# Performance work log

Measured on AMD Instinct MI355X. Metric: run time of the kernel, lower is better.

The kernel has to match this reference:

```python
import jax, jax.numpy as jnp
import numpy as np

DIM = 1024


def setup_inputs() -> dict:
    key = jax.random.key(0)
    ks = jax.random.split(key, 12)
    d = DIM
    B, T = 8, 4096
    s = 1.0 / np.sqrt(d)
    return {
        "x": jax.random.normal(ks[0], (B, T, d), dtype=jnp.float32),
        "u": jnp.ones((d,), dtype=jnp.float32),
        "w": jnp.ones((d,), dtype=jnp.float32),
        "tmk": jnp.ones((d,), dtype=jnp.float32),
        "tmv": jnp.ones((d,), dtype=jnp.float32),
        "tmr": jnp.ones((d,), dtype=jnp.float32),
        "Wk": jax.random.normal(ks[1], (d, d), dtype=jnp.float32) * s,
        "Wv": jax.random.normal(ks[2], (d, d), dtype=jnp.float32) * s,
        "Wr": jax.random.normal(ks[3], (d, d), dtype=jnp.float32) * s,
        "Wo": jax.random.normal(ks[4], (d, d), dtype=jnp.float32) * s,
        "bo": jnp.zeros((d,), dtype=jnp.float32),
    }


def _wkv_scan(k, v, u, w):
    # k, v: [B, T, d]; u, w: [d]
    kT = jnp.swapaxes(k, 0, 1)  # [T, B, d]
    vT = jnp.swapaxes(v, 0, 1)

    def step(carry, kv_t):
        a, b = carry
        k_t, v_t = kv_t
        q = jnp.maximum(u + k_t, w)
        e1 = jnp.exp(-w - q)
        e2 = jnp.exp(u + k_t - q)
        a = e1 * a + e2 * v_t
        b = e1 * b + e2
        return (a, b), a / b

    B, _, d = k.shape
    init = (jnp.zeros((B, d), k.dtype), jnp.zeros((B, d), k.dtype))
    _, wkvT = jax.lax.scan(step, init, (kT, vT))
    return jnp.swapaxes(wkvT, 0, 1)  # [B, T, d]


def reference(x, u, w, tmk, tmv, tmr, Wk, Wv, Wr, Wo, bo):
    # time_shift: zero-pad one step at front, drop last -> x_shifted[t] = x[t-1]
    x_sh = jnp.pad(x, ((0, 0), (1, 0), (0, 0)))[:, :-1, :]
    key = x * tmk + x_sh * (1.0 - tmk)
    value = x * tmv + x_sh * (1.0 - tmv)
    receptance = jax.nn.sigmoid(x * tmr + x_sh * (1.0 - tmr))
    # torch Linear(no bias): y = x @ W.T
    k = jnp.einsum("btd,ed->bte", key, Wk)
    v = jnp.einsum("btd,ed->bte", value, Wv)
    r = jnp.einsum("btd,ed->bte", receptance, Wr)
    wkv = _wkv_scan(k, v, u, w)
    return jnp.einsum("btd,ed->bte", wkv * r, Wo) + bo
```

## Files before the change

kernel.cpp:

```cpp
#include <hip/hip_runtime.h>

#define DIMD 1024
#define BATCH 8
#define SEQ 4096
#define TCH 64
#define NCH (SEQ / TCH)

typedef short short8 __attribute__((ext_vector_type(8)));
typedef unsigned short u16x8 __attribute__((ext_vector_type(8)));
typedef __bf16 bf16x8 __attribute__((ext_vector_type(8)));
typedef float f32x4 __attribute__((ext_vector_type(4)));

static __device__ __forceinline__ unsigned short f2bf(float f) {
    unsigned int u = __builtin_bit_cast(unsigned int, f);
    u += 0x7FFFu + ((u >> 16) & 1u);
    return (unsigned short)(u >> 16);
}
static __device__ __forceinline__ float bf2f(unsigned short s) {
    return __builtin_bit_cast(float, ((unsigned int)s) << 16);
}

__global__ void detect(const unsigned* __restrict__ xw, unsigned* __restrict__ flag) {
    if (threadIdx.x == 0 && blockIdx.x == 0) {
        int cnt = 0;
        for (int i = 0; i < 64; ++i) {
            unsigned lo = xw[i] & 0xFFFFu;
            unsigned e = (lo >> 7) & 0xFFu;
            if ((e >= 0x70u && e <= 0x8Fu) || lo == 0u) ++cnt;
        }
        *flag = (cnt >= 32) ? 1u : 0u;
    }
}

__global__ void cvt_small(const void* __restrict__ s0, const void* __restrict__ s1,
                          const void* __restrict__ s2, const void* __restrict__ s3,
                          const void* __restrict__ s4, const void* __restrict__ s5,
                          float* __restrict__ dst, const unsigned* __restrict__ flag) {
    const void* s;
    switch (blockIdx.y) {
        case 0: s = s0; break; case 1: s = s1; break; case 2: s = s2; break;
        case 3: s = s3; break; case 4: s = s4; break; default: s = s5; break;
    }
    int i = blockIdx.x * 256 + threadIdx.x;
    float v = (*flag) ? bf2f(((const unsigned short*)s)[i]) : ((const float*)s)[i];
    dst[blockIdx.y * 1024 + i] = v;
}

__global__ void cvt_W(const void* __restrict__ s0, const void* __restrict__ s1,
                      const void* __restrict__ s2, const void* __restrict__ s3,
                      unsigned short* __restrict__ dst, const unsigned* __restrict__ flag) {
    const void* s;
    switch (blockIdx.y) {
        case 0: s = s0; break; case 1: s = s1; break;
        case 2: s = s2; break; default: s = s3; break;
    }
    unsigned short* d = dst + (size_t)blockIdx.y * DIMD * DIMD;
    size_t i8 = (size_t)blockIdx.x * 256 + threadIdx.x;
    if (*flag) {
        ((u16x8*)d)[i8] = ((const u16x8*)s)[i8];
    } else {
        const float4* s4 = (const float4*)s;
        float4 a = s4[i8 * 2], b = s4[i8 * 2 + 1];
        u16x8 o;
        o[0] = f2bf(a.x); o[1] = f2bf(a.y); o[2] = f2bf(a.z); o[3] = f2bf(a.w);
        o[4] = f2bf(b.x); o[5] = f2bf(b.y); o[6] = f2bf(b.z); o[7] = f2bf(b.w);
        ((u16x8*)d)[i8] = o;
    }
}

__global__ void prep3(const void* __restrict__ xb, size_t xoff,
                      const float* __restrict__ tmk, const float* __restrict__ tmv,
                      const float* __restrict__ tmr,
                      unsigned short* __restrict__ mix3, size_t mstride,
                      const unsigned* __restrict__ flag) {
    size_t i8 = (size_t)blockIdx.x * 256 + threadIdx.x;
    int d8 = (int)(i8 & 127);
    size_t row = i8 >> 7;
    int t = (int)(row & (SEQ - 1));
    float xv[8], xs[8];
    if (*flag) {
        const unsigned short* x = (const unsigned short*)xb + xoff;
        u16x8 a = ((const u16x8*)x)[i8];
#pragma unroll
        for (int j = 0; j < 8; ++j) xv[j] = bf2f(a[j]);
        if (t > 0) {
            u16x8 b = ((const u16x8*)x)[i8 - 128];
#pragma unroll
            for (int j = 0; j < 8; ++j) xs[j] = bf2f(b[j]);
        } else {
#pragma unroll
            for (int j = 0; j < 8; ++j) xs[j] = 0.f;
        }
    } else {
        const float* x = (const float*)xb + xoff;
        const float4* x4 = (const float4*)x;
        float4 a0 = x4[i8 * 2], a1 = x4[i8 * 2 + 1];
        xv[0]=a0.x; xv[1]=a0.y; xv[2]=a0.z; xv[3]=a0.w;
        xv[4]=a1.x; xv[5]=a1.y; xv[6]=a1.z; xv[7]=a1.w;
        if (t > 0) {
            float4 b0 = x4[i8 * 2 - 256], b1 = x4[i8 * 2 - 255];
            xs[0]=b0.x; xs[1]=b0.y; xs[2]=b0.z; xs[3]=b0.w;
            xs[4]=b1.x; xs[5]=b1.y; xs[6]=b1.z; xs[7]=b1.w;
        } else {
#pragma unroll
            for (int j = 0; j < 8; ++j) xs[j] = 0.f;
        }
    }
    const float4* k4 = (const float4*)tmk;
    const float4* v4 = (const float4*)tmv;
    const float4* r4 = (const float4*)tmr;
    float4 mk0 = k4[d8*2], mk1 = k4[d8*2+1];
    float4 mv0 = v4[d8*2], mv1 = v4[d8*2+1];
    float4 mr0 = r4[d8*2], mr1 = r4[d8*2+1];
    float mk[8] = {mk0.x,mk0.y,mk0.z,mk0.w, mk1.x,mk1.y,mk1.z,mk1.w};
    float mv[8] = {mv0.x,mv0.y,mv0.z,mv0.w, mv1.x,mv1.y,mv1.z,mv1.w};
    float mr[8] = {mr0.x,mr0.y,mr0.z,mr0.w, mr1.x,mr1.y,mr1.z,mr1.w};
    u16x8 ok, ov, orr;
#pragma unroll
    for (int j = 0; j < 8; ++j) {
        float dxy = xv[j] - xs[j];
        ok[j] = f2bf(xs[j] + mk[j] * dxy);
        ov[j] = f2bf(xs[j] + mv[j] * dxy);
        float r = xs[j] + mr[j] * dxy;
        orr[j] = f2bf(1.f / (1.f + __expf(-r)));
    }
    ((u16x8*)(mix3))[i8] = ok;
    ((u16x8*)(mix3 + mstride))[i8] = ov;
    ((u16x8*)(mix3 + 2 * mstride))[i8] = orr;
}

__global__ __launch_bounds__(256) void gemm_fused(
    const unsigned short* __restrict__ Aall,
    const unsigned short* __restrict__ Wall,
    const float* __restrict__ biasf,
    void* __restrict__ Cout, size_t coff,
    int M, int nx, int force_bf16, const unsigned* __restrict__ flag)
{
    __shared__ unsigned short sA[128 * 64];
    __shared__ unsigned short sB[128 * 64];

    const int tid = threadIdx.x;
    const int lane = tid & 63;
    const int wv = tid >> 6;
    const int wm = (wv >> 1) * 64;
    const int wn = (wv & 1) * 64;
    const int l15 = lane & 15;
    const int qd = lane >> 4;

    const int id = blockIdx.x;
    const int cls = id & 7;
    const int sub = id >> 3;
    const int bx = sub % nx;
    const int by = cls + 8 * (sub / nx);
    const int which = bx >> 3;
    const unsigned short* A  = Aall + (size_t)which * M * DIMD;
    const unsigned short* Wp = Wall + (size_t)which * DIMD * DIMD;
    const size_t row0 = (size_t)by * 128;
    const size_t col0 = (size_t)(bx & 7) * 128;

    f32x4 acc[4][4];
#pragma unroll
    for (int i = 0; i < 4; ++i)
#pragma unroll
        for (int j = 0; j < 4; ++j)
            acc[i][j] = {0.f, 0.f, 0.f, 0.f};

    for (int k0 = 0; k0 < DIMD; k0 += 64) {
#pragma unroll
        for (int i = 0; i < 4; ++i) {
            int c = i * 256 + tid;
            int row = c >> 3;
            int jj = c & 7;
            int kA = ((jj ^ (row & 7)) * 8);
            __builtin_amdgcn_global_load_lds(
                (const __attribute__((address_space(1))) void*)(A + (row0 + row) * (size_t)DIMD + k0 + kA),
                (__attribute__((address_space(3))) void*)(sA + c * 8), 16, 0, 0);
            __builtin_amdgcn_global_load_lds(
                (const __attribute__((address_space(1))) void*)(Wp + (col0 + row) * (size_t)DIMD + k0 + kA),
                (__attribute__((address_space(3))) void*)(sB + c * 8), 16, 0, 0);
        }
        __syncthreads();

#pragma unroll
        for (int kh = 0; kh < 2; ++kh) {
            short8 af[4], bfr[4];
#pragma unroll
            for (int mt = 0; mt < 4; ++mt) {
                int r = wm + mt * 16 + l15;
                int j = (kh * 4 + qd) ^ (r & 7);
                af[mt] = *(const short8*)(sA + r * 64 + j * 8);
            }
#pragma unroll
            for (int nt = 0; nt < 4; ++nt) {
                int r = wn + nt * 16 + l15;
                int j = (kh * 4 + qd) ^ (r & 7);
                bfr[nt] = *(const short8*)(sB + r * 64 + j * 8);
            }
#pragma unroll
            for (int mt = 0; mt < 4; ++mt)
#pragma unroll
                for (int nt = 0; nt < 4; ++nt)
                    acc[mt][nt] = __builtin_amdgcn_mfma_f32_16x16x32_bf16(
                        __builtin_bit_cast(bf16x8, af[mt]),
                        __builtin_bit_cast(bf16x8, bfr[nt]),
                        acc[mt][nt], 0, 0, 0);
        }
        __syncthreads();
    }

    const bool wb16 = force_bf16 || (*flag != 0u);
    const size_t cbase = coff + (size_t)which * M * DIMD;
#pragma unroll
    for (int nt = 0; nt < 4; ++nt) {
        size_t gc = col0 + wn + nt * 16 + l15;
        float bv = biasf ? biasf[gc] : 0.f;
#pragma unroll
        for (int mt = 0; mt < 4; ++mt) {
#pragma unroll
            for (int i = 0; i < 4; ++i) {
                size_t gr = row0 + wm + mt * 16 + qd * 4 + i;
                float vvl = acc[mt][nt][i] + bv;
                size_t idx = cbase + gr * (size_t)DIMD + gc;
                if (wb16) ((unsigned short*)Cout)[idx] = f2bf(vvl);
                else      ((float*)Cout)[idx] = vvl;
            }
        }
    }
}

__global__ void wkv_pass1(const unsigned short* __restrict__ kk,
                          const unsigned short* __restrict__ vv,
                          const float* __restrict__ uf, const float* __restrict__ wf,
                          float* __restrict__ aloc, float* __restrict__ bloc,
                          float* __restrict__ pp, int nchan)
{
    int e = blockIdx.x * 256 + threadIdx.x;
    int b = blockIdx.y, c = blockIdx.z;
    float uu = uf[e], ww = wf[e];
    size_t base = ((size_t)(b * SEQ + c * TCH)) * DIMD + e;
    float a = 0.f, bb = 0.f, P = 1.f;
    for (int t = 0; t < TCH; ++t) {
        float kt = bf2f(kk[base + (size_t)t * DIMD]);
        float vt = bf2f(vv[base + (size_t)t * DIMD]);
        float q = fmaxf(uu + kt, ww);
        float e1 = __expf(fminf(-ww - q, 60.f));
        float e2 = __expf(uu + kt - q);
        a = e1 * a + e2 * vt;
        bb = e1 * bb + e2;
        P *= e1;
    }
    P = fminf(fmaxf(P, 0.f), 1e30f);
    size_t si = (size_t)c * nchan + b * DIMD + e;
    aloc[si] = a; bloc[si] = bb; pp[si] = P;
}

__global__ void wkv_pass2(const float* __restrict__ aloc, const float* __restrict__ bloc,
                          const float* __restrict__ pp,
                          float* __restrict__ ain, float* __restrict__ bin, int nchan)
{
    int ch = blockIdx.x * 256 + threadIdx.x;
    float a = 0.f, b = 0.f;
    for (int c = 0; c < NCH; ++c) {
        size_t si = (size_t)c * nchan + ch;
        ain[si] = a; bin[si] = b;
        float P = pp[si];
        a = fmaf(P, a, aloc[si]);
        b = fmaf(P, b, bloc[si]);
    }
}

__global__ void wkv_pass3(const unsigned short* __restrict__ kk,
                          const unsigned short* __restrict__ vv,
                          const unsigned short* __restrict__ rr,
                          const float* __restrict__ uf, const float* __restrict__ wf,
                          const float* __restrict__ ain, const float* __restrict__ bin,
                          unsigned short* __restrict__ ao, int nchan)
{
    int e = blockIdx.x * 256 + threadIdx.x;
    int b = blockIdx.y, c = blockIdx.z;
    float uu = uf[e], ww = wf[e];
    size_t base = ((size_t)(b * SEQ + c * TCH)) * DIMD + e;
    size_t si = (size_t)c * nchan + b * DIMD + e;
    float a = ain[si], bb = bin[si];
    for (int t = 0; t < TCH; ++t) {
        size_t gi = base + (size_t)t * DIMD;
        float kt = bf2f(kk[gi]);
        float vt = bf2f(vv[gi]);
        float q = fmaxf(uu + kt, ww);
        float e1 = __expf(fminf(-ww - q, 60.f));
        float e2 = __expf(uu + kt - q);
        a = e1 * a + e2 * vt;
        bb = e1 * bb + e2;
        float wkv = a / fmaxf(bb, 1e-38f);
        float rv = bf2f(rr[gi]);
        ao[gi] = f2bf(wkv * rv);
    }
}

extern "C" void kernel_launch(void* const* d_in, const int* in_sizes, int n_in,
                              void* d_out, int out_size, void* d_ws, size_t ws_size,
                              hipStream_t stream) {
    const void* x   = d_in[0];
    const void* u   = d_in[1];
    const void* w   = d_in[2];
    const void* tmk = d_in[3];
    const void* tmv = d_in[4];
    const void* tmr = d_in[5];
    const void* Wk  = d_in[6];
    const void* Wv  = d_in[7];
    const void* Wr  = d_in[8];
    const void* Wo  = d_in[9];
    const void* bo  = d_in[10];
    (void)in_sizes; (void)n_in; (void)out_size;

    const size_t MB = 1ull << 20;
    int nb;
    if      (ws_size >= 432 * MB) nb = 8;
    else if (ws_size >= 124 * MB) nb = 2;
    else                          nb = 1;
    const int ngroups = BATCH / nb;
    const size_t Mg = (size_t)nb * SEQ;
    const int nchan = nb * DIMD;

    char* ws = (char*)d_ws;
    unsigned* flag = (unsigned*)(ws);
    float* smallf  = (float*)(ws + 64 * 1024);
    unsigned short* Wb = (unsigned short*)(ws + 1 * MB);
    unsigned short* mix3 = (unsigned short*)(ws + 16 * MB);
    size_t matB = Mg * DIMD * sizeof(unsigned short);
    unsigned short* kvr = (unsigned short*)((char*)mix3 + 3 * matB);
    char* sc = (char*)kvr + 3 * matB;
    size_t scanB = (size_t)NCH * nchan * sizeof(float);
    float* aloc = (float*)(sc + 0 * scanB);
    float* bloc = (float*)(sc + 1 * scanB);
    float* pp   = (float*)(sc + 2 * scanB);
    float* ain  = (float*)(sc + 3 * scanB);
    float* bin  = (float*)(sc + 4 * scanB);

    float* uf   = smallf + 0 * 1024;
    float* wf   = smallf + 1 * 1024;
    float* tmkf = smallf + 2 * 1024;
    float* tmvf = smallf + 3 * 1024;
    float* tmrf = smallf + 4 * 1024;
    float* bof  = smallf + 5 * 1024;
    unsigned short* Wob = Wb + 3ull * DIMD * DIMD;

    detect<<<1, 64, 0, stream>>>((const unsigned*)x, flag);
    cvt_small<<<dim3(4, 6), 256, 0, stream>>>(u, w, tmk, tmv, tmr, bo, smallf, flag);
    cvt_W<<<dim3(512, 4), 256, 0, stream>>>(Wk, Wv, Wr, Wo, Wb, flag);

    const size_t mstride = Mg * DIMD;
    unsigned short* kk  = kvr;
    unsigned short* vvb = kvr + mstride;
    unsigned short* rrb = kvr + 2 * mstride;
    const int ny = (int)(Mg / 128);
    dim3 gScan(DIMD / 256, nb, NCH);

    for (int g = 0; g < ngroups; ++g) {
        size_t xoff = (size_t)g * Mg * DIMD;

        prep3<<<(int)(Mg * DIMD / 8 / 256), 256, 0, stream>>>(
            x, xoff, tmkf, tmvf, tmrf, mix3, mstride, flag);
        gemm_fused<<<24 * ny, 256, 0, stream>>>(
            mix3, Wb, nullptr, kvr, 0, (int)Mg, 24, 1, flag);

        wkv_pass1<<<gScan, 256, 0, stream>>>(kk, vvb, uf, wf, aloc, bloc, pp, nchan);
        wkv_pass2<<<nchan / 256, 256, 0, stream>>>(aloc, bloc, pp, ain, bin, nchan);
        wkv_pass3<<<gScan, 256, 0, stream>>>(kk, vvb, rrb, uf, wf, ain, bin, kk, nchan);

        gemm_fused<<<8 * ny, 256, 0, stream>>>(
            kk, Wob, bof, d_out, xoff, (int)Mg, 8, 0, flag);
    }
}
```

Measured before the change: 811.8 us.

## Rewrite GEMM as 256x256 tile, 8-wave, double-buffered pipelined kernel

```diff
diff --git a/kernel.cpp b/kernel.cpp
--- a/kernel.cpp
+++ b/kernel.cpp
@@ -129,21 +129,75 @@
     ((u16x8*)(mix3 + 2 * mstride))[i8] = orr;
 }
 
-__global__ __launch_bounds__(256) void gemm_fused(
+
+static __device__ __forceinline__ void stage_half(
+    const unsigned short* __restrict__ g, unsigned short* l, int tid)
+{
+#pragma unroll
+    for (int ld = 0; ld < 2; ++ld) {
+        int c = ld * 512 + tid;
+        int row = c >> 3;
+        int jj = c & 7;
+        int kA = (jj ^ (row & 7)) * 8;
+        __builtin_amdgcn_global_load_lds(
+            (const __attribute__((address_space(1))) void*)(g + (size_t)row * DIMD + kA),
+            (__attribute__((address_space(3))) void*)(l + c * 8), 16, 0, 0);
+    }
+}
+
+#define SA_L(buf, h) (lds + (buf) * 16384 + (h) * 8192)
+#define SB_L(buf, h) (lds + 32768 + (buf) * 16384 + (h) * 8192)
+#define STA(buf, h, t) stage_half(A + (row0 + (h) * 128) * DIMD + (t) * 64, SA_L(buf, h), tid)
+#define STB(buf, h, t) stage_half(Wp + (col0 + (h) * 128) * DIMD + (t) * 64, SB_L(buf, h), tid)
+
+#define PH(Q, BUF, STAGES, TAIL)                                                   \
+    {                                                                              \
+        const unsigned short* sAb = lds + (BUF) * 16384;                           \
+        const unsigned short* sBb = lds + 32768 + (BUF) * 16384;                   \
+        short8 af[2][2];                                                           \
+        if ((Q) == 0) {                                                            \
+            _Pragma("unroll") for (int nt = 0; nt < 4; ++nt)                       \
+            _Pragma("unroll") for (int kh = 0; kh < 2; ++kh) {                     \
+                int r = wn + nt * 16 + l15;                                        \
+                int j = (kh * 4 + qd) ^ (r & 7);                                   \
+                bfr[nt][kh] = *(const short8*)(sBb + r * 64 + j * 8);              \
+            }                                                                      \
+        }                                                                          \
+        _Pragma("unroll") for (int m2 = 0; m2 < 2; ++m2)                           \
+        _Pragma("unroll") for (int kh = 0; kh < 2; ++kh) {                         \
+            int r = wm + ((Q) * 2 + m2) * 16 + l15;                                \
+            int j = (kh * 4 + qd) ^ (r & 7);                                       \
+            af[m2][kh] = *(const short8*)(sAb + r * 64 + j * 8);                   \
+        }                                                                          \
+        STAGES;                                                                    \
+        asm volatile("s_barrier" ::: "memory");                                    \
+        __builtin_amdgcn_s_setprio(1);                                             \
+        _Pragma("unroll") for (int m2 = 0; m2 < 2; ++m2)                           \
+        _Pragma("unroll") for (int nt = 0; nt < 4; ++nt)                           \
+        _Pragma("unroll") for (int kh = 0; kh < 2; ++kh)                           \
+            acc[(Q) * 2 + m2][nt] = __builtin_amdgcn_mfma_f32_16x16x32_bf16(       \
+                __builtin_bit_cast(bf16x8, af[m2][kh]),                            \
+                __builtin_bit_cast(bf16x8, bfr[nt][kh]),                           \
+                acc[(Q) * 2 + m2][nt], 0, 0, 0);                                   \
+        __builtin_amdgcn_s_setprio(0);                                             \
+        TAIL;                                                                      \
+        asm volatile("s_barrier" ::: "memory");                                    \
+    }
+
+__global__ __launch_bounds__(512, 2) void gemm_fused(
     const unsigned short* __restrict__ Aall,
     const unsigned short* __restrict__ Wall,
     const float* __restrict__ biasf,
     void* __restrict__ Cout, size_t coff,
     int M, int nx, int force_bf16, const unsigned* __restrict__ flag)
 {
-    __shared__ unsigned short sA[128 * 64];
-    __shared__ unsigned short sB[128 * 64];
+    __shared__ unsigned short lds[65536];
 
     const int tid = threadIdx.x;
     const int lane = tid & 63;
     const int wv = tid >> 6;
-    const int wm = (wv >> 1) * 64;
-    const int wn = (wv & 1) * 64;
+    const int wm = (wv >> 2) * 128;
+    const int wn = (wv & 3) * 64;
     const int l15 = lane & 15;
     const int qd = lane >> 4;
 
@@ -152,77 +206,89 @@
     const int sub = id >> 3;
     const int bx = sub % nx;
     const int by = cls + 8 * (sub / nx);
-    const int which = bx >> 3;
+    const int which = bx >> 2;
     const unsigned short* A  = Aall + (size_t)which * M * DIMD;
     const unsigned short* Wp = Wall + (size_t)which * DIMD * DIMD;
-    const size_t row0 = (size_t)by * 128;
-    const size_t col0 = (size_t)(bx & 7) * 128;
-
-    f32x4 acc[4][4];
-#pragma unroll
-    for (int i = 0; i < 4; ++i)
+    const size_t row0 = (size_t)by * 256;
+    const size_t col0 = (size_t)(bx & 3) * 256;
+
+    f32x4 acc[8][4];
+#pragma unroll
+    for (int i = 0; i < 8; ++i)
 #pragma unroll
         for (int j = 0; j < 4; ++j)
             acc[i][j] = {0.f, 0.f, 0.f, 0.f};
 
-    for (int k0 = 0; k0 < DIMD; k0 += 64) {
-#pragma unroll
-        for (int i = 0; i < 4; ++i) {
-            int c = i * 256 + tid;
-            int row = c >> 3;
-            int jj = c & 7;
-            int kA = ((jj ^ (row & 7)) * 8);
-            __builtin_amdgcn_global_load_lds(
-                (const __attribute__((address_space(1))) void*)(A + (row0 + row) * (size_t)DIMD + k0 + kA),
-                (__attribute__((address_space(3))) void*)(sA + c * 8), 16, 0, 0);
-            __builtin_amdgcn_global_load_lds(
-                (const __attribute__((address_space(1))) void*)(Wp + (col0 + row) * (size_t)DIMD + k0 + kA),
-                (__attribute__((address_space(3))) void*)(sB + c * 8), 16, 0, 0);
-        }
-        __syncthreads();
-
-#pragma unroll
-        for (int kh = 0; kh < 2; ++kh) {
-            short8 af[4], bfr[4];
-#pragma unroll
-            for (int mt = 0; mt < 4; ++mt) {
-                int r = wm + mt * 16 + l15;
-                int j = (kh * 4 + qd) ^ (r & 7);
-                af[mt] = *(const short8*)(sA + r * 64 + j * 8);
-            }
-#pragma unroll
-            for (int nt = 0; nt < 4; ++nt) {
-                int r = wn + nt * 16 + l15;
-                int j = (kh * 4 + qd) ^ (r & 7);
-                bfr[nt] = *(const short8*)(sB + r * 64 + j * 8);
-            }
-#pragma unroll
-            for (int mt = 0; mt < 4; ++mt)
-#pragma unroll
-                for (int nt = 0; nt < 4; ++nt)
-                    acc[mt][nt] = __builtin_amdgcn_mfma_f32_16x16x32_bf16(
-                        __builtin_bit_cast(bf16x8, af[mt]),
-                        __builtin_bit_cast(bf16x8, bfr[nt]),
-                        acc[mt][nt], 0, 0, 0);
-        }
-        __syncthreads();
+    short8 bfr[4][2];
+
+    STB(0, 0, 0); STB(0, 1, 0);
+    STA(0, 0, 0); STA(0, 1, 0);
+    STB(1, 0, 1); STB(1, 1, 1);
+    asm volatile("s_waitcnt vmcnt(4)" ::: "memory");
+    asm volatile("s_barrier" ::: "memory");
+
+    for (int it = 0; it < 8; ++it) {
+        const int o  = 2 * it + 1;
+        const int e2 = 2 * it + 2;
+        const int o2 = 2 * it + 3;
+        const bool pre = (it < 7);
+        PH(0, 0, { STA(1, 0, o); }, {});
+        PH(1, 0, { STA(1, 1, o); }, {});
+        PH(2, 0, { if (pre) STB(0, 0, e2); }, {});
+        PH(3, 0, { if (pre) STB(0, 1, e2); },
+                 { if (pre) { asm volatile("s_waitcnt vmcnt(4)" ::: "memory"); }
+                   else     { asm volatile("s_waitcnt vmcnt(0)" ::: "memory"); } });
+        PH(0, 1, { if (pre) STA(0, 0, e2); }, {});
+        PH(1, 1, { if (pre) STA(0, 1, e2); }, {});
+        PH(2, 1, { if (pre) STB(1, 0, o2); }, {});
+        PH(3, 1, { if (pre) STB(1, 1, o2); },
+                 { if (pre) { asm volatile("s_waitcnt vmcnt(4)" ::: "memory"); } });
     }
 
     const bool wb16 = force_bf16 || (*flag != 0u);
     const size_t cbase = coff + (size_t)which * M * DIMD;
-#pragma unroll
-    for (int nt = 0; nt < 4; ++nt) {
-        size_t gc = col0 + wn + nt * 16 + l15;
-        float bv = biasf ? biasf[gc] : 0.f;
-#pragma unroll
-        for (int mt = 0; mt < 4; ++mt) {
+    if (wb16) {
+        unsigned short* sC = lds;
+        float bvv[4];
+#pragma unroll
+        for (int nt = 0; nt < 4; ++nt)
+            bvv[nt] = biasf ? biasf[col0 + wn + nt * 16 + l15] : 0.f;
+#pragma unroll
+        for (int mt = 0; mt < 8; ++mt)
+#pragma unroll
+        for (int nt = 0; nt < 4; ++nt)
+#pragma unroll
+        for (int i = 0; i < 4; ++i) {
+            int row = wm + mt * 16 + qd * 4 + i;
+            int col = wn + nt * 16 + l15;
+            int j = col >> 3;
+            int js = j ^ (((row >> 2) & 3) << 1);
+            sC[row * 256 + js * 8 + (col & 7)] = f2bf(acc[mt][nt][i] + bvv[nt]);
+        }
+        __syncthreads();
+        unsigned short* Cb = (unsigned short*)Cout;
+#pragma unroll
+        for (int ch = 0; ch < 16; ++ch) {
+            int c = ch * 512 + tid;
+            int row = c >> 5;
+            int jj = c & 31;
+            int js = jj ^ (((row >> 2) & 3) << 1);
+            short8 vv = *(const short8*)(sC + row * 256 + js * 8);
+            *(u16x8*)(Cb + cbase + (row0 + row) * DIMD + col0 + jj * 8) =
+                __builtin_bit_cast(u16x8, vv);
+        }
+    } else {
+        float* Cf = (float*)Cout;
+#pragma unroll
+        for (int nt = 0; nt < 4; ++nt) {
+            size_t gc = col0 + wn + nt * 16 + l15;
+            float bv = biasf ? biasf[gc] : 0.f;
+#pragma unroll
+            for (int mt = 0; mt < 8; ++mt)
 #pragma unroll
             for (int i = 0; i < 4; ++i) {
                 size_t gr = row0 + wm + mt * 16 + qd * 4 + i;
-                float vvl = acc[mt][nt][i] + bv;
-                size_t idx = cbase + gr * (size_t)DIMD + gc;
-                if (wb16) ((unsigned short*)Cout)[idx] = f2bf(vvl);
-                else      ((float*)Cout)[idx] = vvl;
+                Cf[cbase + gr * DIMD + gc] = acc[mt][nt][i] + bv;
             }
         }
     }
@@ -353,7 +419,7 @@
     unsigned short* kk  = kvr;
     unsigned short* vvb = kvr + mstride;
     unsigned short* rrb = kvr + 2 * mstride;
-    const int ny = (int)(Mg / 128);
+    const int ny = (int)(Mg / 256);
     dim3 gScan(DIMD / 256, nb, NCH);
 
     for (int g = 0; g < ngroups; ++g) {
@@ -361,14 +427,14 @@
 
         prep3<<<(int)(Mg * DIMD / 8 / 256), 256, 0, stream>>>(
             x, xoff, tmkf, tmvf, tmrf, mix3, mstride, flag);
-        gemm_fused<<<24 * ny, 256, 0, stream>>>(
-            mix3, Wb, nullptr, kvr, 0, (int)Mg, 24, 1, flag);
+        gemm_fused<<<12 * ny, 512, 0, stream>>>(
+            mix3, Wb, nullptr, kvr, 0, (int)Mg, 12, 1, flag);
 
         wkv_pass1<<<gScan, 256, 0, stream>>>(kk, vvb, uf, wf, aloc, bloc, pp, nchan);
         wkv_pass2<<<nchan / 256, 256, 0, stream>>>(aloc, bloc, pp, ain, bin, nchan);
         wkv_pass3<<<gScan, 256, 0, stream>>>(kk, vvb, rrb, uf, wf, ain, bin, kk, nchan);
 
-        gemm_fused<<<8 * ny, 256, 0, stream>>>(
-            kk, Wob, bof, d_out, xoff, (int)Mg, 8, 0, flag);
-    }
-}
+        gemm_fused<<<4 * ny, 512, 0, stream>>>(
+            kk, Wob, bof, d_out, xoff, (int)Mg, 4, 0, flag);
+    }
+}
```

New measurement: 651.3 us. -19.8%, faster.
